# Optimization experiments

Hardware: AMD Instinct MI355X
Metric: run time of the kernel (lower is better)

Reference implementation:

```python
import jax, jax.numpy as jnp
import numpy as np

N_NODES = 100000
N_EDGES = 1600000
IN_CH, HID_CH, OUT_CH = 128, 128, 64


def setup_inputs() -> dict:
    key = jax.random.key(0)
    ks = jax.random.split(key, 9)
    x = jax.random.normal(ks[0], (N_NODES, IN_CH), dtype=jnp.float32)
    edge_index = jax.random.randint(ks[1], (2, N_EDGES), 0, N_NODES, dtype=jnp.int64)
    def glorot(k, shape):
        fan_in = shape[1]
        return jax.random.normal(k, shape, dtype=jnp.float32) / jnp.sqrt(jnp.float32(fan_in))
    return {
        "x": x,
        "edge_index": edge_index,
        "W1_l": glorot(ks[2], (HID_CH, IN_CH)),
        "W1_r": glorot(ks[3], (HID_CH, IN_CH)),
        "b1": jnp.zeros((HID_CH,), jnp.float32),
        "W2_l": glorot(ks[4], (HID_CH, HID_CH)),
        "W2_r": glorot(ks[5], (HID_CH, HID_CH)),
        "b2": jnp.zeros((HID_CH,), jnp.float32),
        "W3_l": glorot(ks[6], (OUT_CH, HID_CH)),
        "W3_r": glorot(ks[7], (OUT_CH, HID_CH)),
        "b3": jnp.zeros((OUT_CH,), jnp.float32),
    }


def _sage_conv(x, src, dst, W_l, W_r, b):
    # PyG SAGEConv (aggr='mean', root_weight=True): out = lin_l(mean_j x_j) + lin_r(x_i)
    n = x.shape[0]
    msg = x[src]                                            # [E, C] gather at source
    agg = jax.ops.segment_sum(msg, dst, num_segments=n)     # [N, C] scatter-sum at dest
    cnt = jax.ops.segment_sum(jnp.ones((src.shape[0],), x.dtype), dst, num_segments=n)
    mean = agg / jnp.maximum(cnt, 1.0)[:, None]             # zero-in-degree nodes -> 0
    return mean @ W_l.T + x @ W_r.T + b


def reference(x, edge_index, W1_l, W1_r, b1, W2_l, W2_r, b2, W3_l, W3_r, b3):
    src, dst = edge_index[0], edge_index[1]
    h = jax.nn.relu(_sage_conv(x, src, dst, W1_l, W1_r, b1))
    # F.dropout with training=False is identity (eval mode)
    h = jax.nn.relu(_sage_conv(h, src, dst, W2_l, W2_r, b2))
    return _sage_conv(h, src, dst, W3_l, W3_r, b3)
```

## Files before the change

kernel.cpp:

```cpp
#include <hip/hip_runtime.h>
#include <hip/hip_bf16.h>
#include <cstddef>
#include <cstdint>

#define NBLK(n, b) (((n) + (b) - 1) / (b))

typedef __attribute__((ext_vector_type(8))) short short8;
typedef __attribute__((ext_vector_type(4))) float f32x4;

__device__ inline unsigned short f2bf(float f) {
  union { float f; unsigned u; } v; v.f = f;
  unsigned u = v.u;
  u += 0x7FFFu + ((u >> 16) & 1u);
  return (unsigned short)(u >> 16);
}
__device__ inline float bflo(unsigned u) { union { unsigned u; float f; } v; v.u = u << 16; return v.f; }
__device__ inline float bfhi(unsigned u) { union { unsigned u; float f; } v; v.u = u & 0xFFFF0000u; return v.f; }

#define BSHIFT 9
#define BSIZE 512
#define CAPSHIFT 14
#define CAP 16384
#define ECHUNK 2048

__global__ __launch_bounds__(256) void k_cast(
    const float* __restrict__ x, unsigned* __restrict__ xb, int N,
    const float* __restrict__ W1l, const float* __restrict__ W1r, unsigned short* __restrict__ Wb1,
    const float* __restrict__ W2l, const float* __restrict__ W2r, unsigned short* __restrict__ Wb2,
    const float* __restrict__ W3l, const float* __restrict__ W3r, unsigned short* __restrict__ Wb3) {
  int t = threadIdx.x;
  int b = blockIdx.x;
  int gCast = (N * 64 + 255) >> 8;
  if (b < gCast) {
    int i = b * 256 + t;
    if (i < N * 64) {
      float2 v = *(const float2*)(x + (size_t)i * 2);
      xb[i] = (unsigned)f2bf(v.x) | ((unsigned)f2bf(v.y) << 16);
    }
    return;
  }
  b -= gCast;
  int ii = b * 256 + t;
  const float *Wl, *Wr; unsigned short* Wb;
  if (ii < 128 * 256) { Wl = W1l; Wr = W1r; Wb = Wb1; }
  else if (ii < 256 * 256) { Wl = W2l; Wr = W2r; Wb = Wb2; ii -= 128 * 256; }
  else { Wl = W3l; Wr = W3r; Wb = Wb3; ii -= 256 * 256; }
  int nrow = ii >> 8, k = ii & 255;
  float v = (k < 128) ? Wr[nrow * 128 + k] : Wl[nrow * 128 + (k - 128)];
  Wb[ii] = f2bf(v);
}

__global__ __launch_bounds__(256) void k_scatter(
    const void* __restrict__ edges, int* __restrict__ bucketCursor,
    unsigned* __restrict__ bucketed, int E, int NB) {
  __shared__ int h[1024];
  __shared__ int base2[1024];
  int t = threadIdx.x;
  int b = blockIdx.x;

  const unsigned* e32 = (const unsigned*)edges;
  int is64 = 1;
#pragma unroll
  for (int i = 0; i < 16; ++i)
    if (e32[2 * i + 1] != 0u) is64 = 0;

  for (int i = t; i < NB; i += 256) h[i] = 0;
  __syncthreads();
  int base_e = b * ECHUNK;
  unsigned key[8];
  int bkt[8];
#pragma unroll
  for (int k = 0; k < 8; ++k) {
    int e = base_e + k * 256 + t;
    bkt[k] = -1;
    if (e < E) {
      int s, d;
      if (is64) {
        s = (int)((const long long*)edges)[e];
        d = (int)((const long long*)edges)[(size_t)E + e];
      } else {
        s = ((const int*)edges)[e];
        d = ((const int*)edges)[(size_t)E + e];
      }
      bkt[k] = d >> BSHIFT;
      key[k] = (unsigned)s | ((unsigned)(d & (BSIZE - 1)) << 17);
      atomicAdd(&h[bkt[k]], 1);
    }
  }
  __syncthreads();
  for (int i = t; i < NB; i += 256) {
    int c = h[i];
    base2[i] = c ? atomicAdd(&bucketCursor[i], c) : 0;
    h[i] = 0;
  }
  __syncthreads();
#pragma unroll
  for (int k = 0; k < 8; ++k) {
    if (bkt[k] >= 0) {
      int r = atomicAdd(&h[bkt[k]], 1);
      int pos = base2[bkt[k]] + r;
      if (pos < CAP)
        bucketed[((size_t)bkt[k] << CAPSHIFT) + pos] = key[k];
    }
  }
}

__global__ __launch_bounds__(256) void k_csr(const unsigned* __restrict__ bucketed,
                                             const int* __restrict__ bucketCursor,
                                             int* __restrict__ rowStart, int* __restrict__ deg,
                                             int* __restrict__ srcSorted, int N, int NB) {
  __shared__ int h[512];
  __shared__ int excl[512];
  __shared__ int sd[256];
  int b = blockIdx.x;
  int t = threadIdx.x;
  int nodeBase = b << BSHIFT;
  int nNode = min(BSIZE, N - nodeBase);
  int cnt = min(bucketCursor[b], CAP);
  size_t s0 = (size_t)b << CAPSHIFT;
  h[t * 2] = 0; h[t * 2 + 1] = 0;
  __syncthreads();
  for (int i = t; i < cnt; i += 256) {
    int ld = bucketed[s0 + i] >> 17;
    atomicAdd(&h[ld], 1);
  }
  __syncthreads();
  int a0 = h[t * 2], a1 = h[t * 2 + 1];
  int s = a0 + a1;
  sd[t] = s;
  __syncthreads();
  for (int off = 1; off < 256; off <<= 1) {
    int xv = (t >= off) ? sd[t - off] : 0;
    __syncthreads();
    sd[t] += xv;
    __syncthreads();
  }
  int run = sd[t] - s;
  excl[t * 2] = run;
  excl[t * 2 + 1] = run + a0;
  if (t * 2 < nNode) {
    rowStart[nodeBase + t * 2] = (int)s0 + run;
    deg[nodeBase + t * 2] = a0;
  }
  if (t * 2 + 1 < nNode) {
    rowStart[nodeBase + t * 2 + 1] = (int)s0 + run + a0;
    deg[nodeBase + t * 2 + 1] = a1;
  }
  h[t * 2] = 0; h[t * 2 + 1] = 0;
  __syncthreads();
  for (int i = t; i < cnt; i += 256) {
    unsigned u = bucketed[s0 + i];
    int ld = u >> 17;
    int r = atomicAdd(&h[ld], 1);
    srcSorted[s0 + excl[ld] + r] = (int)(u & 0x1FFFFu);
  }
}

__global__ void k_aggregate(const unsigned* __restrict__ in, const int* __restrict__ rowStart,
                            const int* __restrict__ deg, const int* __restrict__ srcs,
                            unsigned* __restrict__ mean, int n) {
  int lane = threadIdx.x & 63;
  int w = threadIdx.x >> 6;
  int node = blockIdx.x * 4 + w;
  if (node >= n) return;
  int r0 = rowStart[node];
  int dg = deg[node];
  int r1 = r0 + dg;
  int sub = lane & 15;
  int eg = lane >> 4;
  float acc[8];
#pragma unroll
  for (int k = 0; k < 8; ++k) acc[k] = 0.f;

  for (int base = r0; base < r1; base += 64) {
    int e = base + lane;
    int sv = (e < r1) ? srcs[e] : 0;
    int cnt = min(64, r1 - base);
    int j = 0;
    for (; j + 16 <= cnt; j += 16) {
      int s0 = __shfl(sv, j + eg);
      int s1 = __shfl(sv, j + 4 + eg);
      int s2 = __shfl(sv, j + 8 + eg);
      int s3 = __shfl(sv, j + 12 + eg);
      uint4 u0 = *(const uint4*)(in + (size_t)s0 * 64 + sub * 4);
      uint4 u1 = *(const uint4*)(in + (size_t)s1 * 64 + sub * 4);
      uint4 u2 = *(const uint4*)(in + (size_t)s2 * 64 + sub * 4);
      uint4 u3 = *(const uint4*)(in + (size_t)s3 * 64 + sub * 4);
      acc[0] += bflo(u0.x); acc[1] += bfhi(u0.x);
      acc[2] += bflo(u0.y); acc[3] += bfhi(u0.y);
      acc[4] += bflo(u0.z); acc[5] += bfhi(u0.z);
      acc[6] += bflo(u0.w); acc[7] += bfhi(u0.w);
      acc[0] += bflo(u1.x); acc[1] += bfhi(u1.x);
      acc[2] += bflo(u1.y); acc[3] += bfhi(u1.y);
      acc[4] += bflo(u1.z); acc[5] += bfhi(u1.z);
      acc[6] += bflo(u1.w); acc[7] += bfhi(u1.w);
      acc[0] += bflo(u2.x); acc[1] += bfhi(u2.x);
      acc[2] += bflo(u2.y); acc[3] += bfhi(u2.y);
      acc[4] += bflo(u2.z); acc[5] += bfhi(u2.z);
      acc[6] += bflo(u2.w); acc[7] += bfhi(u2.w);
      acc[0] += bflo(u3.x); acc[1] += bfhi(u3.x);
      acc[2] += bflo(u3.y); acc[3] += bfhi(u3.y);
      acc[4] += bflo(u3.z); acc[5] += bfhi(u3.z);
      acc[6] += bflo(u3.w); acc[7] += bfhi(u3.w);
    }
    for (; j + 8 <= cnt; j += 8) {
      int s0 = __shfl(sv, j + eg);
      int s1 = __shfl(sv, j + 4 + eg);
      uint4 u0 = *(const uint4*)(in + (size_t)s0 * 64 + sub * 4);
      uint4 u1 = *(const uint4*)(in + (size_t)s1 * 64 + sub * 4);
      acc[0] += bflo(u0.x); acc[1] += bfhi(u0.x);
      acc[2] += bflo(u0.y); acc[3] += bfhi(u0.y);
      acc[4] += bflo(u0.z); acc[5] += bfhi(u0.z);
      acc[6] += bflo(u0.w); acc[7] += bfhi(u0.w);
      acc[0] += bflo(u1.x); acc[1] += bfhi(u1.x);
      acc[2] += bflo(u1.y); acc[3] += bfhi(u1.y);
      acc[4] += bflo(u1.z); acc[5] += bfhi(u1.z);
      acc[6] += bflo(u1.w); acc[7] += bfhi(u1.w);
    }
    for (; j < cnt; j += 4) {
      int jj = j + eg;
      int s = __shfl(sv, jj);
      if (jj < cnt) {
        uint4 u = *(const uint4*)(in + (size_t)s * 64 + sub * 4);
        acc[0] += bflo(u.x); acc[1] += bfhi(u.x);
        acc[2] += bflo(u.y); acc[3] += bfhi(u.y);
        acc[4] += bflo(u.z); acc[5] += bfhi(u.z);
        acc[6] += bflo(u.w); acc[7] += bfhi(u.w);
      }
    }
  }

#pragma unroll
  for (int k = 0; k < 8; ++k) {
    acc[k] += __shfl_down(acc[k], 32);
    acc[k] += __shfl_down(acc[k], 16);
  }
  if (eg == 0) {
    float sc = 1.0f / (float)max(dg, 1);
    uint4 o;
    o.x = (unsigned)f2bf(acc[0] * sc) | ((unsigned)f2bf(acc[1] * sc) << 16);
    o.y = (unsigned)f2bf(acc[2] * sc) | ((unsigned)f2bf(acc[3] * sc) << 16);
    o.z = (unsigned)f2bf(acc[4] * sc) | ((unsigned)f2bf(acc[5] * sc) << 16);
    o.w = (unsigned)f2bf(acc[6] * sc) | ((unsigned)f2bf(acc[7] * sc) << 16);
    *(uint4*)(mean + (size_t)node * 64 + sub * 4) = o;
  }
}

template <int H, bool RELU, bool BF16OUT>
__global__ __launch_bounds__(256) void k_gemm(
    const unsigned short* __restrict__ selfB, const unsigned short* __restrict__ meanB,
    const unsigned short* __restrict__ Wb, const float* __restrict__ bias,
    void* __restrict__ outp, int n) {
  constexpr int TN = H / 32;
  int lane = threadIdx.x & 63;
  int w = threadIdx.x >> 6;
  int wr = w & 1, wc = w >> 1;
  int nodeBase = blockIdx.x * 128 + wr * 64;
  int colBase = wc * (H / 2);
  int l15 = lane & 15, quad = lane >> 4;

  f32x4 acc[4][TN];
#pragma unroll
  for (int t = 0; t < 4; ++t)
#pragma unroll
    for (int j = 0; j < TN; ++j) acc[t][j] = (f32x4){0.f, 0.f, 0.f, 0.f};

#pragma unroll
  for (int c = 0; c < 8; ++c) {
    const unsigned short* A = (c < 4) ? selfB : meanB;
    int ko = (c & 3) * 32 + quad * 8;
    short8 af[4], bfr[TN];
#pragma unroll
    for (int t = 0; t < 4; ++t) {
      int row = min(nodeBase + t * 16 + l15, n - 1);
      af[t] = *(const short8*)(A + (size_t)row * 128 + ko);
    }
#pragma unroll
    for (int j = 0; j < TN; ++j) {
      int cn = colBase + j * 16 + l15;
      bfr[j] = *(const short8*)(Wb + (size_t)cn * 256 + c * 32 + quad * 8);
    }
#pragma unroll
    for (int t = 0; t < 4; ++t)
#pragma unroll
      for (int j = 0; j < TN; ++j)
        acc[t][j] = __builtin_amdgcn_mfma_f32_16x16x32_bf16(af[t], bfr[j], acc[t][j], 0, 0, 0);
  }

#pragma unroll
  for (int j = 0; j < TN; ++j) {
    int col = colBase + j * 16 + l15;
    float bv = bias[col];
#pragma unroll
    for (int t = 0; t < 4; ++t) {
#pragma unroll
      for (int r = 0; r < 4; ++r) {
        int row = nodeBase + t * 16 + quad * 4 + r;
        if (row < n) {
          float v = acc[t][j][r] + bv;
          if (RELU) v = fmaxf(v, 0.f);
          if (BF16OUT) ((unsigned short*)outp)[(size_t)row * H + col] = f2bf(v);
          else ((float*)outp)[(size_t)row * H + col] = v;
        }
      }
    }
  }
}

__global__ __launch_bounds__(256) void k_gemm3_both(
    const unsigned short* __restrict__ A,
    const unsigned short* __restrict__ Wb3,
    const float* __restrict__ bias,
    float* __restrict__ outp, unsigned short* __restrict__ y3, int n) {
  int lane = threadIdx.x & 63;
  int w = threadIdx.x >> 6;
  int wr = w & 1, wc = w >> 1;
  int nodeBase = blockIdx.x * 128 + wr * 64;
  int l15 = lane & 15, quad = lane >> 4;
  int woff = wc ? 128 : 0;
  f32x4 acc[4][4];
#pragma unroll
  for (int t = 0; t < 4; ++t)
#pragma unroll
    for (int j = 0; j < 4; ++j) acc[t][j] = (f32x4){0.f, 0.f, 0.f, 0.f};
#pragma unroll
  for (int c = 0; c < 4; ++c) {
    int ko = c * 32 + quad * 8;
    short8 af[4], bfr[4];
#pragma unroll
    for (int t = 0; t < 4; ++t) {
      int row = min(nodeBase + t * 16 + l15, n - 1);
      af[t] = *(const short8*)(A + (size_t)row * 128 + ko);
    }
#pragma unroll
    for (int j = 0; j < 4; ++j) {
      int cn = j * 16 + l15;
      bfr[j] = *(const short8*)(Wb3 + (size_t)cn * 256 + woff + c * 32 + quad * 8);
    }
#pragma unroll
    for (int t = 0; t < 4; ++t)
#pragma unroll
      for (int j = 0; j < 4; ++j)
        acc[t][j] = __builtin_amdgcn_mfma_f32_16x16x32_bf16(af[t], bfr[j], acc[t][j], 0, 0, 0);
  }
#pragma unroll
  for (int j = 0; j < 4; ++j) {
    int col = j * 16 + l15;
    float bv = wc ? 0.f : bias[col];
#pragma unroll
    for (int t = 0; t < 4; ++t) {
#pragma unroll
      for (int r = 0; r < 4; ++r) {
        int row = nodeBase + t * 16 + quad * 4 + r;
        if (row < n) {
          float v = acc[t][j][r] + bv;
          if (wc) y3[(size_t)row * 64 + col] = f2bf(v);
          else outp[(size_t)row * 64 + col] = v;
        }
      }
    }
  }
}

__global__ void k_agg64_add(const unsigned* __restrict__ y3, const int* __restrict__ rowStart,
                            const int* __restrict__ deg, const int* __restrict__ srcs,
                            float* __restrict__ outp, int n) {
  int lane = threadIdx.x & 63;
  int w = threadIdx.x >> 6;
  int node = blockIdx.x * 4 + w;
  if (node >= n) return;
  int dg = deg[node];
  if (dg == 0) return;
  int r0 = rowStart[node];
  int r1 = r0 + dg;
  int sub = lane & 7;
  int eg = lane >> 3;
  float acc[8];
#pragma unroll
  for (int k = 0; k < 8; ++k) acc[k] = 0.f;

  for (int base = r0; base < r1; base += 64) {
    int e = base + lane;
    int sv = (e < r1) ? srcs[e] : 0;
    int cnt = min(64, r1 - base);
    int j = 0;
    for (; j + 16 <= cnt; j += 16) {
      int s0 = __shfl(sv, j + eg);
      int s1 = __shfl(sv, j + 8 + eg);
      uint4 u0 = *(const uint4*)(y3 + (size_t)s0 * 32 + sub * 4);
      uint4 u1 = *(const uint4*)(y3 + (size_t)s1 * 32 + sub * 4);
      acc[0] += bflo(u0.x); acc[1] += bfhi(u0.x);
      acc[2] += bflo(u0.y); acc[3] += bfhi(u0.y);
      acc[4] += bflo(u0.z); acc[5] += bfhi(u0.z);
      acc[6] += bflo(u0.w); acc[7] += bfhi(u0.w);
      acc[0] += bflo(u1.x); acc[1] += bfhi(u1.x);
      acc[2] += bflo(u1.y); acc[3] += bfhi(u1.y);
      acc[4] += bflo(u1.z); acc[5] += bfhi(u1.z);
      acc[6] += bflo(u1.w); acc[7] += bfhi(u1.w);
    }
    for (; j < cnt; j += 8) {
      int jj = j + eg;
      int s = __shfl(sv, jj);
      if (jj < cnt) {
        uint4 u = *(const uint4*)(y3 + (size_t)s * 32 + sub * 4);
        acc[0] += bflo(u.x); acc[1] += bfhi(u.x);
        acc[2] += bflo(u.y); acc[3] += bfhi(u.y);
        acc[4] += bflo(u.z); acc[5] += bfhi(u.z);
        acc[6] += bflo(u.w); acc[7] += bfhi(u.w);
      }
    }
  }

#pragma unroll
  for (int k = 0; k < 8; ++k) {
    acc[k] += __shfl_down(acc[k], 32);
    acc[k] += __shfl_down(acc[k], 16);
    acc[k] += __shfl_down(acc[k], 8);
  }
  if (eg == 0) {
    float sc = 1.0f / (float)dg;
    float* op = outp + (size_t)node * 64 + sub * 8;
    float4 a = *(float4*)op;
    float4 b = *(float4*)(op + 4);
    a.x += acc[0] * sc; a.y += acc[1] * sc; a.z += acc[2] * sc; a.w += acc[3] * sc;
    b.x += acc[4] * sc; b.y += acc[5] * sc; b.z += acc[6] * sc; b.w += acc[7] * sc;
    *(float4*)op = a;
    *(float4*)(op + 4) = b;
  }
}


extern "C" void kernel_launch(void* const* d_in, const int* in_sizes, int n_in,
                              void* d_out, int out_size, void* d_ws, size_t ws_size,
                              hipStream_t stream) {
  (void)n_in; (void)out_size; (void)ws_size;
  const float* x = (const float*)d_in[0];
  const void* edges = d_in[1];
  const float* W1l = (const float*)d_in[2];
  const float* W1r = (const float*)d_in[3];
  const float* b1 = (const float*)d_in[4];
  const float* W2l = (const float*)d_in[5];
  const float* W2r = (const float*)d_in[6];
  const float* b2 = (const float*)d_in[7];
  const float* W3l = (const float*)d_in[8];
  const float* W3r = (const float*)d_in[9];
  const float* b3 = (const float*)d_in[10];
  float* out = (float*)d_out;

  const int N = in_sizes[0] / 128;
  const int E = in_sizes[1] / 2;
  const int NB = (N + BSIZE - 1) >> BSHIFT;

  char* ws = (char*)d_ws;
  size_t off = 0;
  auto alloc = [&](size_t bytes) -> char* {
    char* p = ws + off;
    off = (off + bytes + 255) & ~(size_t)255;
    return p;
  };
  int* bucketCursor = (int*)alloc((size_t)NB * 4);
  unsigned* bucketed = (unsigned*)alloc((size_t)NB * CAP * 4);
  int* rowStart = (int*)alloc((size_t)N * 4);
  int* deg = (int*)alloc((size_t)N * 4);
  int* srcSorted = (int*)alloc((size_t)NB * CAP * 4);
  unsigned short* xb = (unsigned short*)alloc((size_t)N * 128 * 2);
  unsigned short* mean = (unsigned short*)alloc((size_t)N * 128 * 2);
  unsigned short* h1 = (unsigned short*)alloc((size_t)N * 128 * 2);
  unsigned short* h2 = (unsigned short*)alloc((size_t)N * 128 * 2);
  unsigned short* y3 = (unsigned short*)alloc((size_t)N * 64 * 2);
  unsigned short* Wb1 = (unsigned short*)alloc(128 * 256 * 2);
  unsigned short* Wb2 = (unsigned short*)alloc(128 * 256 * 2);
  unsigned short* Wb3 = (unsigned short*)alloc(64 * 256 * 2);

  int gCast = NBLK(N * 64, 256) + 320;
  int gE = NBLK(E, ECHUNK);
  int gAgg = NBLK(N, 4);
  int gGemm = NBLK(N, 128);

  hipMemsetAsync(bucketCursor, 0, (size_t)NB * 4, stream);
  k_cast<<<gCast, 256, 0, stream>>>(x, (unsigned*)xb, N,
                                    W1l, W1r, Wb1, W2l, W2r, Wb2, W3l, W3r, Wb3);
  k_scatter<<<gE, 256, 0, stream>>>(edges, bucketCursor, bucketed, E, NB);
  k_csr<<<NB, 256, 0, stream>>>(bucketed, bucketCursor, rowStart, deg, srcSorted, N, NB);

  k_aggregate<<<gAgg, 256, 0, stream>>>((const unsigned*)xb, rowStart, deg, srcSorted, (unsigned*)mean, N);
  k_gemm<128, true, true><<<gGemm, 256, 0, stream>>>(xb, mean, Wb1, b1, h1, N);
  k_aggregate<<<gAgg, 256, 0, stream>>>((const unsigned*)h1, rowStart, deg, srcSorted, (unsigned*)mean, N);
  k_gemm<128, true, true><<<gGemm, 256, 0, stream>>>(h1, mean, Wb2, b2, h2, N);
  k_gemm3_both<<<gGemm, 256, 0, stream>>>(h2, Wb3, b3, out, y3, N);
  k_agg64_add<<<gAgg, 256, 0, stream>>>((const unsigned*)y3, rowStart, deg, srcSorted, out, N);
}
```

Baseline: 459.0 us.

## Store features in channel-sliced layout and aggregate per slice with thread-per-node

Feature matrices are stored as 8 (or 4) column slices of 16 bf16 channels, each slice contiguous over nodes. Aggregation now launches one block per node range and slice, and each thread pair gathers 32-byte slice rows for one node with 8 loads in flight. The goal is to keep each slice's working set (about 3.2 MB) cache-resident during random gathers and to remove the wave-wide shuffles and reductions. The trade-off is that each thread walks its node's full edge list serially, so load imbalance grows, and the GEMM A-loads and stores become strided across slices.

```diff
diff --git a/kernel.cpp b/kernel.cpp
--- a/kernel.cpp
+++ b/kernel.cpp
@@ -7,6 +7,7 @@
 
 typedef __attribute__((ext_vector_type(8))) short short8;
 typedef __attribute__((ext_vector_type(4))) float f32x4;
+typedef __attribute__((ext_vector_type(2))) float f32x2;
 
 __device__ inline unsigned short f2bf(float f) {
   union { float f; unsigned u; } v; v.f = f;
@@ -23,8 +24,9 @@
 #define CAP 16384
 #define ECHUNK 2048
 
+
 __global__ __launch_bounds__(256) void k_cast(
-    const float* __restrict__ x, unsigned* __restrict__ xb, int N,
+    const float* __restrict__ x, unsigned* __restrict__ xT, int N,
     const float* __restrict__ W1l, const float* __restrict__ W1r, unsigned short* __restrict__ Wb1,
     const float* __restrict__ W2l, const float* __restrict__ W2r, unsigned short* __restrict__ Wb2,
     const float* __restrict__ W3l, const float* __restrict__ W3r, unsigned short* __restrict__ Wb3) {
@@ -35,7 +37,9 @@
     int i = b * 256 + t;
     if (i < N * 64) {
       float2 v = *(const float2*)(x + (size_t)i * 2);
-      xb[i] = (unsigned)f2bf(v.x) | ((unsigned)f2bf(v.y) << 16);
+      int node = i >> 6, j = i & 63;
+      xT[((size_t)(j >> 3) * N + node) * 8 + (j & 7)] =
+          (unsigned)f2bf(v.x) | ((unsigned)f2bf(v.y) << 16);
     }
     return;
   }
@@ -156,101 +160,53 @@
   }
 }
 
-__global__ void k_aggregate(const unsigned* __restrict__ in, const int* __restrict__ rowStart,
-                            const int* __restrict__ deg, const int* __restrict__ srcs,
-                            unsigned* __restrict__ mean, int n) {
-  int lane = threadIdx.x & 63;
-  int w = threadIdx.x >> 6;
-  int node = blockIdx.x * 4 + w;
+__global__ __launch_bounds__(256) void k_agg_slice(
+    const uint4* __restrict__ inT, const int* __restrict__ rowStart,
+    const int* __restrict__ deg, const int* __restrict__ srcs,
+    uint4* __restrict__ outT, int n) {
+  int g = blockIdx.x & 7;
+  int node = ((blockIdx.x >> 3) << 7) + (threadIdx.x >> 1);
+  int h = threadIdx.x & 1;
   if (node >= n) return;
-  int r0 = rowStart[node];
   int dg = deg[node];
-  int r1 = r0 + dg;
-  int sub = lane & 15;
-  int eg = lane >> 4;
-  float acc[8];
-#pragma unroll
-  for (int k = 0; k < 8; ++k) acc[k] = 0.f;
-
-  for (int base = r0; base < r1; base += 64) {
-    int e = base + lane;
-    int sv = (e < r1) ? srcs[e] : 0;
-    int cnt = min(64, r1 - base);
-    int j = 0;
-    for (; j + 16 <= cnt; j += 16) {
-      int s0 = __shfl(sv, j + eg);
-      int s1 = __shfl(sv, j + 4 + eg);
-      int s2 = __shfl(sv, j + 8 + eg);
-      int s3 = __shfl(sv, j + 12 + eg);
-      uint4 u0 = *(const uint4*)(in + (size_t)s0 * 64 + sub * 4);
-      uint4 u1 = *(const uint4*)(in + (size_t)s1 * 64 + sub * 4);
-      uint4 u2 = *(const uint4*)(in + (size_t)s2 * 64 + sub * 4);
-      uint4 u3 = *(const uint4*)(in + (size_t)s3 * 64 + sub * 4);
-      acc[0] += bflo(u0.x); acc[1] += bfhi(u0.x);
-      acc[2] += bflo(u0.y); acc[3] += bfhi(u0.y);
-      acc[4] += bflo(u0.z); acc[5] += bfhi(u0.z);
-      acc[6] += bflo(u0.w); acc[7] += bfhi(u0.w);
-      acc[0] += bflo(u1.x); acc[1] += bfhi(u1.x);
-      acc[2] += bflo(u1.y); acc[3] += bfhi(u1.y);
-      acc[4] += bflo(u1.z); acc[5] += bfhi(u1.z);
-      acc[6] += bflo(u1.w); acc[7] += bfhi(u1.w);
-      acc[0] += bflo(u2.x); acc[1] += bfhi(u2.x);
-      acc[2] += bflo(u2.y); acc[3] += bfhi(u2.y);
-      acc[4] += bflo(u2.z); acc[5] += bfhi(u2.z);
-      acc[6] += bflo(u2.w); acc[7] += bfhi(u2.w);
-      acc[0] += bflo(u3.x); acc[1] += bfhi(u3.x);
-      acc[2] += bflo(u3.y); acc[3] += bfhi(u3.y);
-      acc[4] += bflo(u3.z); acc[5] += bfhi(u3.z);
-      acc[6] += bflo(u3.w); acc[7] += bfhi(u3.w);
-    }
-    for (; j + 8 <= cnt; j += 8) {
-      int s0 = __shfl(sv, j + eg);
-      int s1 = __shfl(sv, j + 4 + eg);
-      uint4 u0 = *(const uint4*)(in + (size_t)s0 * 64 + sub * 4);
-      uint4 u1 = *(const uint4*)(in + (size_t)s1 * 64 + sub * 4);
-      acc[0] += bflo(u0.x); acc[1] += bfhi(u0.x);
-      acc[2] += bflo(u0.y); acc[3] += bfhi(u0.y);
-      acc[4] += bflo(u0.z); acc[5] += bfhi(u0.z);
-      acc[6] += bflo(u0.w); acc[7] += bfhi(u0.w);
-      acc[0] += bflo(u1.x); acc[1] += bfhi(u1.x);
-      acc[2] += bflo(u1.y); acc[3] += bfhi(u1.y);
-      acc[4] += bflo(u1.z); acc[5] += bfhi(u1.z);
-      acc[6] += bflo(u1.w); acc[7] += bfhi(u1.w);
-    }
-    for (; j < cnt; j += 4) {
-      int jj = j + eg;
-      int s = __shfl(sv, jj);
-      if (jj < cnt) {
-        uint4 u = *(const uint4*)(in + (size_t)s * 64 + sub * 4);
-        acc[0] += bflo(u.x); acc[1] += bfhi(u.x);
-        acc[2] += bflo(u.y); acc[3] += bfhi(u.y);
-        acc[4] += bflo(u.z); acc[5] += bfhi(u.z);
-        acc[6] += bflo(u.w); acc[7] += bfhi(u.w);
+  f32x2 acc0 = {0.f, 0.f}, acc1 = {0.f, 0.f}, acc2 = {0.f, 0.f}, acc3 = {0.f, 0.f};
+  const uint4* base = inT + (size_t)g * n * 2 + h;
+  if (dg > 0) {
+    int r0 = rowStart[node];
+    int r1 = r0 + dg;
+    for (int b = r0; b < r1; b += 8) {
+      int s[8];
+      uint4 v[8];
+#pragma unroll
+      for (int i = 0; i < 8; ++i) s[i] = srcs[min(b + i, r1 - 1)] & 0x1FFFF;
+#pragma unroll
+      for (int i = 0; i < 8; ++i) v[i] = base[(size_t)s[i] * 2];
+#pragma unroll
+      for (int i = 0; i < 8; ++i) {
+        if (b + i < r1) {
+          f32x2 t0 = {bflo(v[i].x), bfhi(v[i].x)};
+          f32x2 t1 = {bflo(v[i].y), bfhi(v[i].y)};
+          f32x2 t2 = {bflo(v[i].z), bfhi(v[i].z)};
+          f32x2 t3 = {bflo(v[i].w), bfhi(v[i].w)};
+          acc0 += t0; acc1 += t1; acc2 += t2; acc3 += t3;
+        }
       }
     }
   }
-
-#pragma unroll
-  for (int k = 0; k < 8; ++k) {
-    acc[k] += __shfl_down(acc[k], 32);
-    acc[k] += __shfl_down(acc[k], 16);
-  }
-  if (eg == 0) {
-    float sc = 1.0f / (float)max(dg, 1);
-    uint4 o;
-    o.x = (unsigned)f2bf(acc[0] * sc) | ((unsigned)f2bf(acc[1] * sc) << 16);
-    o.y = (unsigned)f2bf(acc[2] * sc) | ((unsigned)f2bf(acc[3] * sc) << 16);
-    o.z = (unsigned)f2bf(acc[4] * sc) | ((unsigned)f2bf(acc[5] * sc) << 16);
-    o.w = (unsigned)f2bf(acc[6] * sc) | ((unsigned)f2bf(acc[7] * sc) << 16);
-    *(uint4*)(mean + (size_t)node * 64 + sub * 4) = o;
-  }
-}
-
-template <int H, bool RELU, bool BF16OUT>
+  float sc = 1.0f / (float)max(dg, 1);
+  uint4 o;
+  o.x = (unsigned)f2bf(acc0.x * sc) | ((unsigned)f2bf(acc0.y * sc) << 16);
+  o.y = (unsigned)f2bf(acc1.x * sc) | ((unsigned)f2bf(acc1.y * sc) << 16);
+  o.z = (unsigned)f2bf(acc2.x * sc) | ((unsigned)f2bf(acc2.y * sc) << 16);
+  o.w = (unsigned)f2bf(acc3.x * sc) | ((unsigned)f2bf(acc3.y * sc) << 16);
+  outT[((size_t)g * n + node) * 2 + h] = o;
+}
+
+template <int H, bool RELU>
 __global__ __launch_bounds__(256) void k_gemm(
-    const unsigned short* __restrict__ selfB, const unsigned short* __restrict__ meanB,
+    const unsigned short* __restrict__ selfT, const unsigned short* __restrict__ meanT,
     const unsigned short* __restrict__ Wb, const float* __restrict__ bias,
-    void* __restrict__ outp, int n) {
+    unsigned short* __restrict__ outT, int n) {
   constexpr int TN = H / 32;
   int lane = threadIdx.x & 63;
   int w = threadIdx.x >> 6;
@@ -267,13 +223,15 @@
 
 #pragma unroll
   for (int c = 0; c < 8; ++c) {
-    const unsigned short* A = (c < 4) ? selfB : meanB;
+    const unsigned short* A = (c < 4) ? selfT : meanT;
     int ko = (c & 3) * 32 + quad * 8;
+    int gk = ko >> 4;
+    int wo = ko & 15;
     short8 af[4], bfr[TN];
 #pragma unroll
     for (int t = 0; t < 4; ++t) {
       int row = min(nodeBase + t * 16 + l15, n - 1);
-      af[t] = *(const short8*)(A + (size_t)row * 128 + ko);
+      af[t] = *(const short8*)(A + ((size_t)gk * n + row) * 16 + wo);
     }
 #pragma unroll
     for (int j = 0; j < TN; ++j) {
@@ -290,6 +248,7 @@
 #pragma unroll
   for (int j = 0; j < TN; ++j) {
     int col = colBase + j * 16 + l15;
+    int gc = col >> 4;
     float bv = bias[col];
 #pragma unroll
     for (int t = 0; t < 4; ++t) {
@@ -299,8 +258,7 @@
         if (row < n) {
           float v = acc[t][j][r] + bv;
           if (RELU) v = fmaxf(v, 0.f);
-          if (BF16OUT) ((unsigned short*)outp)[(size_t)row * H + col] = f2bf(v);
-          else ((float*)outp)[(size_t)row * H + col] = v;
+          outT[((size_t)gc * n + row) * 16 + l15] = f2bf(v);
         }
       }
     }
@@ -311,7 +269,7 @@
     const unsigned short* __restrict__ A,
     const unsigned short* __restrict__ Wb3,
     const float* __restrict__ bias,
-    float* __restrict__ outp, unsigned short* __restrict__ y3, int n) {
+    float* __restrict__ outp, unsigned short* __restrict__ y3T, int n) {
   int lane = threadIdx.x & 63;
   int w = threadIdx.x >> 6;
   int wr = w & 1, wc = w >> 1;
@@ -326,11 +284,13 @@
 #pragma unroll
   for (int c = 0; c < 4; ++c) {
     int ko = c * 32 + quad * 8;
+    int gk = ko >> 4;
+    int wo = ko & 15;
     short8 af[4], bfr[4];
 #pragma unroll
     for (int t = 0; t < 4; ++t) {
       int row = min(nodeBase + t * 16 + l15, n - 1);
-      af[t] = *(const short8*)(A + (size_t)row * 128 + ko);
+      af[t] = *(const short8*)(A + ((size_t)gk * n + row) * 16 + wo);
     }
 #pragma unroll
     for (int j = 0; j < 4; ++j) {
@@ -354,7 +314,7 @@
         int row = nodeBase + t * 16 + quad * 4 + r;
         if (row < n) {
           float v = acc[t][j][r] + bv;
-          if (wc) y3[(size_t)row * 64 + col] = f2bf(v);
+          if (wc) y3T[((size_t)j * n + row) * 16 + l15] = f2bf(v);
           else outp[(size_t)row * 64 + col] = v;
         }
       }
@@ -362,71 +322,46 @@
   }
 }
 
-__global__ void k_agg64_add(const unsigned* __restrict__ y3, const int* __restrict__ rowStart,
-                            const int* __restrict__ deg, const int* __restrict__ srcs,
-                            float* __restrict__ outp, int n) {
-  int lane = threadIdx.x & 63;
-  int w = threadIdx.x >> 6;
-  int node = blockIdx.x * 4 + w;
+__global__ __launch_bounds__(256) void k_agg64_slice(
+    const uint4* __restrict__ y3T, const int* __restrict__ rowStart,
+    const int* __restrict__ deg, const int* __restrict__ srcs,
+    float* __restrict__ outp, int n) {
+  int g = blockIdx.x & 3;
+  int node = ((blockIdx.x >> 2) << 7) + (threadIdx.x >> 1);
+  int h = threadIdx.x & 1;
   if (node >= n) return;
   int dg = deg[node];
   if (dg == 0) return;
   int r0 = rowStart[node];
   int r1 = r0 + dg;
-  int sub = lane & 7;
-  int eg = lane >> 3;
-  float acc[8];
-#pragma unroll
-  for (int k = 0; k < 8; ++k) acc[k] = 0.f;
-
-  for (int base = r0; base < r1; base += 64) {
-    int e = base + lane;
-    int sv = (e < r1) ? srcs[e] : 0;
-    int cnt = min(64, r1 - base);
-    int j = 0;
-    for (; j + 16 <= cnt; j += 16) {
-      int s0 = __shfl(sv, j + eg);
-      int s1 = __shfl(sv, j + 8 + eg);
-      uint4 u0 = *(const uint4*)(y3 + (size_t)s0 * 32 + sub * 4);
-      uint4 u1 = *(const uint4*)(y3 + (size_t)s1 * 32 + sub * 4);
-      acc[0] += bflo(u0.x); acc[1] += bfhi(u0.x);
-      acc[2] += bflo(u0.y); acc[3] += bfhi(u0.y);
-      acc[4] += bflo(u0.z); acc[5] += bfhi(u0.z);
-      acc[6] += bflo(u0.w); acc[7] += bfhi(u0.w);
-      acc[0] += bflo(u1.x); acc[1] += bfhi(u1.x);
-      acc[2] += bflo(u1.y); acc[3] += bfhi(u1.y);
-      acc[4] += bflo(u1.z); acc[5] += bfhi(u1.z);
-      acc[6] += bflo(u1.w); acc[7] += bfhi(u1.w);
-    }
-    for (; j < cnt; j += 8) {
-      int jj = j + eg;
-      int s = __shfl(sv, jj);
-      if (jj < cnt) {
-        uint4 u = *(const uint4*)(y3 + (size_t)s * 32 + sub * 4);
-        acc[0] += bflo(u.x); acc[1] += bfhi(u.x);
-        acc[2] += bflo(u.y); acc[3] += bfhi(u.y);
-        acc[4] += bflo(u.z); acc[5] += bfhi(u.z);
-        acc[6] += bflo(u.w); acc[7] += bfhi(u.w);
+  f32x2 acc0 = {0.f, 0.f}, acc1 = {0.f, 0.f}, acc2 = {0.f, 0.f}, acc3 = {0.f, 0.f};
+  const uint4* base = y3T + (size_t)g * n * 2 + h;
+  for (int b = r0; b < r1; b += 8) {
+    int s[8];
+    uint4 v[8];
+#pragma unroll
+    for (int i = 0; i < 8; ++i) s[i] = srcs[min(b + i, r1 - 1)] & 0x1FFFF;
+#pragma unroll
+    for (int i = 0; i < 8; ++i) v[i] = base[(size_t)s[i] * 2];
+#pragma unroll
+    for (int i = 0; i < 8; ++i) {
+      if (b + i < r1) {
+        f32x2 t0 = {bflo(v[i].x), bfhi(v[i].x)};
+        f32x2 t1 = {bflo(v[i].y), bfhi(v[i].y)};
+        f32x2 t2 = {bflo(v[i].z), bfhi(v[i].z)};
+        f32x2 t3 = {bflo(v[i].w), bfhi(v[i].w)};
+        acc0 += t0; acc1 += t1; acc2 += t2; acc3 += t3;
       }
     }
   }
-
-#pragma unroll
-  for (int k = 0; k < 8; ++k) {
-    acc[k] += __shfl_down(acc[k], 32);
-    acc[k] += __shfl_down(acc[k], 16);
-    acc[k] += __shfl_down(acc[k], 8);
-  }
-  if (eg == 0) {
-    float sc = 1.0f / (float)dg;
-    float* op = outp + (size_t)node * 64 + sub * 8;
-    float4 a = *(float4*)op;
-    float4 b = *(float4*)(op + 4);
-    a.x += acc[0] * sc; a.y += acc[1] * sc; a.z += acc[2] * sc; a.w += acc[3] * sc;
-    b.x += acc[4] * sc; b.y += acc[5] * sc; b.z += acc[6] * sc; b.w += acc[7] * sc;
-    *(float4*)op = a;
-    *(float4*)(op + 4) = b;
-  }
+  float sc = 1.0f / (float)dg;
+  float* op = outp + (size_t)node * 64 + g * 16 + h * 8;
+  float4 a = *(float4*)op;
+  float4 c = *(float4*)(op + 4);
+  a.x += acc0.x * sc; a.y += acc0.y * sc; a.z += acc1.x * sc; a.w += acc1.y * sc;
+  c.x += acc2.x * sc; c.y += acc2.y * sc; c.z += acc3.x * sc; c.w += acc3.y * sc;
+  *(float4*)op = a;
+  *(float4*)(op + 4) = c;
 }
 
 
@@ -463,30 +398,33 @@
   int* rowStart = (int*)alloc((size_t)N * 4);
   int* deg = (int*)alloc((size_t)N * 4);
   int* srcSorted = (int*)alloc((size_t)NB * CAP * 4);
-  unsigned short* xb = (unsigned short*)alloc((size_t)N * 128 * 2);
-  unsigned short* mean = (unsigned short*)alloc((size_t)N * 128 * 2);
-  unsigned short* h1 = (unsigned short*)alloc((size_t)N * 128 * 2);
-  unsigned short* h2 = (unsigned short*)alloc((size_t)N * 128 * 2);
-  unsigned short* y3 = (unsigned short*)alloc((size_t)N * 64 * 2);
+  unsigned short* xT = (unsigned short*)alloc((size_t)N * 128 * 2);
+  unsigned short* meanT = (unsigned short*)alloc((size_t)N * 128 * 2);
+  unsigned short* h1T = (unsigned short*)alloc((size_t)N * 128 * 2);
+  unsigned short* h2T = (unsigned short*)alloc((size_t)N * 128 * 2);
+  unsigned short* y3T = (unsigned short*)alloc((size_t)N * 64 * 2);
   unsigned short* Wb1 = (unsigned short*)alloc(128 * 256 * 2);
   unsigned short* Wb2 = (unsigned short*)alloc(128 * 256 * 2);
   unsigned short* Wb3 = (unsigned short*)alloc(64 * 256 * 2);
 
   int gCast = NBLK(N * 64, 256) + 320;
   int gE = NBLK(E, ECHUNK);
-  int gAgg = NBLK(N, 4);
+  int gRange = NBLK(N, 128);
   int gGemm = NBLK(N, 128);
 
   hipMemsetAsync(bucketCursor, 0, (size_t)NB * 4, stream);
-  k_cast<<<gCast, 256, 0, stream>>>(x, (unsigned*)xb, N,
+  k_cast<<<gCast, 256, 0, stream>>>(x, (unsigned*)xT, N,
                                     W1l, W1r, Wb1, W2l, W2r, Wb2, W3l, W3r, Wb3);
   k_scatter<<<gE, 256, 0, stream>>>(edges, bucketCursor, bucketed, E, NB);
   k_csr<<<NB, 256, 0, stream>>>(bucketed, bucketCursor, rowStart, deg, srcSorted, N, NB);
 
-  k_aggregate<<<gAgg, 256, 0, stream>>>((const unsigned*)xb, rowStart, deg, srcSorted, (unsigned*)mean, N);
-  k_gemm<128, true, true><<<gGemm, 256, 0, stream>>>(xb, mean, Wb1, b1, h1, N);
-  k_aggregate<<<gAgg, 256, 0, stream>>>((const unsigned*)h1, rowStart, deg, srcSorted, (unsigned*)mean, N);
-  k_gemm<128, true, true><<<gGemm, 256, 0, stream>>>(h1, mean, Wb2, b2, h2, N);
-  k_gemm3_both<<<gGemm, 256, 0, stream>>>(h2, Wb3, b3, out, y3, N);
-  k_agg64_add<<<gAgg, 256, 0, stream>>>((const unsigned*)y3, rowStart, deg, srcSorted, out, N);
-}
+  k_agg_slice<<<gRange * 8, 256, 0, stream>>>((const uint4*)xT, rowStart, deg, srcSorted,
+                                              (uint4*)meanT, N);
+  k_gemm<128, true><<<gGemm, 256, 0, stream>>>(xT, meanT, Wb1, b1, h1T, N);
+  k_agg_slice<<<gRange * 8, 256, 0, stream>>>((const uint4*)h1T, rowStart, deg, srcSorted,
+                                              (uint4*)meanT, N);
+  k_gemm<128, true><<<gGemm, 256, 0, stream>>>(h1T, meanT, Wb2, b2, h2T, N);
+  k_gemm3_both<<<gGemm, 256, 0, stream>>>(h2T, Wb3, b3, out, y3T, N);
+  k_agg64_slice<<<gRange * 4, 256, 0, stream>>>((const uint4*)y3T, rowStart, deg, srcSorted,
+                                                out, N);
+}
```

After: 525.0 us. +14.4%, slower.

## Degree-sort nodes per bucket and aggregate two nodes per wavefront

Applied to the files above, without the earlier changes.

The CSR build kernel now also emits a permutation that orders nodes within each 512-node bucket by in-degree (capped at 63) using a shared-memory counting sort. The aggregation kernels read this permutation and let each wavefront process two nodes of similar degree together, issuing their gathers interleaved. This is meant to cut load imbalance and raise memory-level parallelism. The cost is an extra indirection, more registers per wave, and scattered output writes in permuted order.

```diff
diff --git a/kernel.cpp b/kernel.cpp
--- a/kernel.cpp
+++ b/kernel.cpp
@@ -16,6 +16,14 @@
 }
 __device__ inline float bflo(unsigned u) { union { unsigned u; float f; } v; v.u = u << 16; return v.f; }
 __device__ inline float bfhi(unsigned u) { union { unsigned u; float f; } v; v.u = u & 0xFFFF0000u; return v.f; }
+
+__device__ inline void add8(float* a, uint4 v) {
+  a[0] += bflo(v.x); a[1] += bfhi(v.x);
+  a[2] += bflo(v.y); a[3] += bfhi(v.y);
+  a[4] += bflo(v.z); a[5] += bfhi(v.z);
+  a[6] += bflo(v.w); a[7] += bfhi(v.w);
+}
+
 
 #define BSHIFT 9
 #define BSIZE 512
@@ -108,7 +116,8 @@
 __global__ __launch_bounds__(256) void k_csr(const unsigned* __restrict__ bucketed,
                                              const int* __restrict__ bucketCursor,
                                              int* __restrict__ rowStart, int* __restrict__ deg,
-                                             int* __restrict__ srcSorted, int N, int NB) {
+                                             int* __restrict__ srcSorted, int* __restrict__ perm,
+                                             int N, int NB) {
   __shared__ int h[512];
   __shared__ int excl[512];
   __shared__ int sd[256];
@@ -154,95 +163,146 @@
     int r = atomicAdd(&h[ld], 1);
     srcSorted[s0 + excl[ld] + r] = (int)(u & 0x1FFFFu);
   }
+  __syncthreads();
+  if (t < 64) sd[t] = 0;
+  __syncthreads();
+  if (t * 2 < nNode) atomicAdd(&sd[min(a0, 63)], 1);
+  if (t * 2 + 1 < nNode) atomicAdd(&sd[min(a1, 63)], 1);
+  __syncthreads();
+  if (t == 0) {
+    int r2 = 0;
+    for (int i = 0; i < 64; ++i) { int c = sd[i]; excl[i] = r2; r2 += c; }
+  }
+  __syncthreads();
+  if (t * 2 < nNode) {
+    int p = atomicAdd(&excl[min(a0, 63)], 1);
+    perm[nodeBase + p] = nodeBase + t * 2;
+  }
+  if (t * 2 + 1 < nNode) {
+    int p = atomicAdd(&excl[min(a1, 63)], 1);
+    perm[nodeBase + p] = nodeBase + t * 2 + 1;
+  }
 }
 
 __global__ void k_aggregate(const unsigned* __restrict__ in, const int* __restrict__ rowStart,
                             const int* __restrict__ deg, const int* __restrict__ srcs,
-                            unsigned* __restrict__ mean, int n) {
+                            const int* __restrict__ perm, unsigned* __restrict__ mean, int n) {
   int lane = threadIdx.x & 63;
   int w = threadIdx.x >> 6;
-  int node = blockIdx.x * 4 + w;
-  if (node >= n) return;
-  int r0 = rowStart[node];
-  int dg = deg[node];
-  int r1 = r0 + dg;
+  int i0 = blockIdx.x * 8 + w * 2;
+  bool vA = i0 < n, vB = i0 + 1 < n;
+  int nA = vA ? perm[i0] : 0;
+  int nB = vB ? perm[i0 + 1] : 0;
+  int dga = vA ? deg[nA] : 0;
+  int dgb = vB ? deg[nB] : 0;
+  int r0a = vA ? rowStart[nA] : 0;
+  int r0b = vB ? rowStart[nB] : 0;
   int sub = lane & 15;
   int eg = lane >> 4;
-  float acc[8];
-#pragma unroll
-  for (int k = 0; k < 8; ++k) acc[k] = 0.f;
-
-  for (int base = r0; base < r1; base += 64) {
-    int e = base + lane;
-    int sv = (e < r1) ? srcs[e] : 0;
-    int cnt = min(64, r1 - base);
+  float accA[8], accB[8];
+#pragma unroll
+  for (int k = 0; k < 8; ++k) { accA[k] = 0.f; accB[k] = 0.f; }
+
+  int mx = max(dga, dgb);
+  for (int base = 0; base < mx; base += 64) {
+    int cA = min(64, dga - base);
+    int cB = min(64, dgb - base);
+    int svA = (lane < cA) ? srcs[r0a + base + lane] : 0;
+    int svB = (lane < cB) ? srcs[r0b + base + lane] : 0;
     int j = 0;
-    for (; j + 16 <= cnt; j += 16) {
-      int s0 = __shfl(sv, j + eg);
-      int s1 = __shfl(sv, j + 4 + eg);
-      int s2 = __shfl(sv, j + 8 + eg);
-      int s3 = __shfl(sv, j + 12 + eg);
-      uint4 u0 = *(const uint4*)(in + (size_t)s0 * 64 + sub * 4);
-      uint4 u1 = *(const uint4*)(in + (size_t)s1 * 64 + sub * 4);
-      uint4 u2 = *(const uint4*)(in + (size_t)s2 * 64 + sub * 4);
-      uint4 u3 = *(const uint4*)(in + (size_t)s3 * 64 + sub * 4);
-      acc[0] += bflo(u0.x); acc[1] += bfhi(u0.x);
-      acc[2] += bflo(u0.y); acc[3] += bfhi(u0.y);
-      acc[4] += bflo(u0.z); acc[5] += bfhi(u0.z);
-      acc[6] += bflo(u0.w); acc[7] += bfhi(u0.w);
-      acc[0] += bflo(u1.x); acc[1] += bfhi(u1.x);
-      acc[2] += bflo(u1.y); acc[3] += bfhi(u1.y);
-      acc[4] += bflo(u1.z); acc[5] += bfhi(u1.z);
-      acc[6] += bflo(u1.w); acc[7] += bfhi(u1.w);
-      acc[0] += bflo(u2.x); acc[1] += bfhi(u2.x);
-      acc[2] += bflo(u2.y); acc[3] += bfhi(u2.y);
-      acc[4] += bflo(u2.z); acc[5] += bfhi(u2.z);
-      acc[6] += bflo(u2.w); acc[7] += bfhi(u2.w);
-      acc[0] += bflo(u3.x); acc[1] += bfhi(u3.x);
-      acc[2] += bflo(u3.y); acc[3] += bfhi(u3.y);
-      acc[4] += bflo(u3.z); acc[5] += bfhi(u3.z);
-      acc[6] += bflo(u3.w); acc[7] += bfhi(u3.w);
-    }
-    for (; j + 8 <= cnt; j += 8) {
-      int s0 = __shfl(sv, j + eg);
-      int s1 = __shfl(sv, j + 4 + eg);
-      uint4 u0 = *(const uint4*)(in + (size_t)s0 * 64 + sub * 4);
-      uint4 u1 = *(const uint4*)(in + (size_t)s1 * 64 + sub * 4);
-      acc[0] += bflo(u0.x); acc[1] += bfhi(u0.x);
-      acc[2] += bflo(u0.y); acc[3] += bfhi(u0.y);
-      acc[4] += bflo(u0.z); acc[5] += bfhi(u0.z);
-      acc[6] += bflo(u0.w); acc[7] += bfhi(u0.w);
-      acc[0] += bflo(u1.x); acc[1] += bfhi(u1.x);
-      acc[2] += bflo(u1.y); acc[3] += bfhi(u1.y);
-      acc[4] += bflo(u1.z); acc[5] += bfhi(u1.z);
-      acc[6] += bflo(u1.w); acc[7] += bfhi(u1.w);
-    }
-    for (; j < cnt; j += 4) {
-      int jj = j + eg;
-      int s = __shfl(sv, jj);
-      if (jj < cnt) {
-        uint4 u = *(const uint4*)(in + (size_t)s * 64 + sub * 4);
-        acc[0] += bflo(u.x); acc[1] += bfhi(u.x);
-        acc[2] += bflo(u.y); acc[3] += bfhi(u.y);
-        acc[4] += bflo(u.z); acc[5] += bfhi(u.z);
-        acc[6] += bflo(u.w); acc[7] += bfhi(u.w);
+    int cM = min(cA, cB);
+    for (; j + 16 <= cM; j += 16) {
+      int a0 = __shfl(svA, j + eg), a1 = __shfl(svA, j + 4 + eg);
+      int a2 = __shfl(svA, j + 8 + eg), a3 = __shfl(svA, j + 12 + eg);
+      int b0 = __shfl(svB, j + eg), b1 = __shfl(svB, j + 4 + eg);
+      int b2 = __shfl(svB, j + 8 + eg), b3 = __shfl(svB, j + 12 + eg);
+      uint4 uA0 = *(const uint4*)(in + (size_t)a0 * 64 + sub * 4);
+      uint4 uA1 = *(const uint4*)(in + (size_t)a1 * 64 + sub * 4);
+      uint4 uA2 = *(const uint4*)(in + (size_t)a2 * 64 + sub * 4);
+      uint4 uA3 = *(const uint4*)(in + (size_t)a3 * 64 + sub * 4);
+      uint4 uB0 = *(const uint4*)(in + (size_t)b0 * 64 + sub * 4);
+      uint4 uB1 = *(const uint4*)(in + (size_t)b1 * 64 + sub * 4);
+      uint4 uB2 = *(const uint4*)(in + (size_t)b2 * 64 + sub * 4);
+      uint4 uB3 = *(const uint4*)(in + (size_t)b3 * 64 + sub * 4);
+      add8(accA, uA0); add8(accA, uA1); add8(accA, uA2); add8(accA, uA3);
+      add8(accB, uB0); add8(accB, uB1); add8(accB, uB2); add8(accB, uB3);
+    }
+    int ja = j;
+    for (; ja + 16 <= cA; ja += 16) {
+      int a0 = __shfl(svA, ja + eg), a1 = __shfl(svA, ja + 4 + eg);
+      int a2 = __shfl(svA, ja + 8 + eg), a3 = __shfl(svA, ja + 12 + eg);
+      uint4 u0 = *(const uint4*)(in + (size_t)a0 * 64 + sub * 4);
+      uint4 u1 = *(const uint4*)(in + (size_t)a1 * 64 + sub * 4);
+      uint4 u2 = *(const uint4*)(in + (size_t)a2 * 64 + sub * 4);
+      uint4 u3 = *(const uint4*)(in + (size_t)a3 * 64 + sub * 4);
+      add8(accA, u0); add8(accA, u1); add8(accA, u2); add8(accA, u3);
+    }
+    for (; ja + 8 <= cA; ja += 8) {
+      int a0 = __shfl(svA, ja + eg), a1 = __shfl(svA, ja + 4 + eg);
+      uint4 u0 = *(const uint4*)(in + (size_t)a0 * 64 + sub * 4);
+      uint4 u1 = *(const uint4*)(in + (size_t)a1 * 64 + sub * 4);
+      add8(accA, u0); add8(accA, u1);
+    }
+    for (; ja < cA; ja += 4) {
+      int jj = ja + eg;
+      int s2 = __shfl(svA, jj);
+      if (jj < cA) {
+        uint4 u = *(const uint4*)(in + (size_t)s2 * 64 + sub * 4);
+        add8(accA, u);
+      }
+    }
+    int jb = j;
+    for (; jb + 16 <= cB; jb += 16) {
+      int b0 = __shfl(svB, jb + eg), b1 = __shfl(svB, jb + 4 + eg);
+      int b2 = __shfl(svB, jb + 8 + eg), b3 = __shfl(svB, jb + 12 + eg);
+      uint4 u0 = *(const uint4*)(in + (size_t)b0 * 64 + sub * 4);
+      uint4 u1 = *(const uint4*)(in + (size_t)b1 * 64 + sub * 4);
+      uint4 u2 = *(const uint4*)(in + (size_t)b2 * 64 + sub * 4);
+      uint4 u3 = *(const uint4*)(in + (size_t)b3 * 64 + sub * 4);
+      add8(accB, u0); add8(accB, u1); add8(accB, u2); add8(accB, u3);
+    }
+    for (; jb + 8 <= cB; jb += 8) {
+      int b0 = __shfl(svB, jb + eg), b1 = __shfl(svB, jb + 4 + eg);
+      uint4 u0 = *(const uint4*)(in + (size_t)b0 * 64 + sub * 4);
+      uint4 u1 = *(const uint4*)(in + (size_t)b1 * 64 + sub * 4);
+      add8(accB, u0); add8(accB, u1);
+    }
+    for (; jb < cB; jb += 4) {
+      int jj = jb + eg;
+      int s2 = __shfl(svB, jj);
+      if (jj < cB) {
+        uint4 u = *(const uint4*)(in + (size_t)s2 * 64 + sub * 4);
+        add8(accB, u);
       }
     }
   }
 
 #pragma unroll
   for (int k = 0; k < 8; ++k) {
-    acc[k] += __shfl_down(acc[k], 32);
-    acc[k] += __shfl_down(acc[k], 16);
+    accA[k] += __shfl_down(accA[k], 32);
+    accA[k] += __shfl_down(accA[k], 16);
+    accB[k] += __shfl_down(accB[k], 32);
+    accB[k] += __shfl_down(accB[k], 16);
   }
   if (eg == 0) {
-    float sc = 1.0f / (float)max(dg, 1);
-    uint4 o;
-    o.x = (unsigned)f2bf(acc[0] * sc) | ((unsigned)f2bf(acc[1] * sc) << 16);
-    o.y = (unsigned)f2bf(acc[2] * sc) | ((unsigned)f2bf(acc[3] * sc) << 16);
-    o.z = (unsigned)f2bf(acc[4] * sc) | ((unsigned)f2bf(acc[5] * sc) << 16);
-    o.w = (unsigned)f2bf(acc[6] * sc) | ((unsigned)f2bf(acc[7] * sc) << 16);
-    *(uint4*)(mean + (size_t)node * 64 + sub * 4) = o;
+    if (vA) {
+      float sc = 1.0f / (float)max(dga, 1);
+      uint4 o;
+      o.x = (unsigned)f2bf(accA[0] * sc) | ((unsigned)f2bf(accA[1] * sc) << 16);
+      o.y = (unsigned)f2bf(accA[2] * sc) | ((unsigned)f2bf(accA[3] * sc) << 16);
+      o.z = (unsigned)f2bf(accA[4] * sc) | ((unsigned)f2bf(accA[5] * sc) << 16);
+      o.w = (unsigned)f2bf(accA[6] * sc) | ((unsigned)f2bf(accA[7] * sc) << 16);
+      *(uint4*)(mean + (size_t)nA * 64 + sub * 4) = o;
+    }
+    if (vB) {
+      float sc = 1.0f / (float)max(dgb, 1);
+      uint4 o;
+      o.x = (unsigned)f2bf(accB[0] * sc) | ((unsigned)f2bf(accB[1] * sc) << 16);
+      o.y = (unsigned)f2bf(accB[2] * sc) | ((unsigned)f2bf(accB[3] * sc) << 16);
+      o.z = (unsigned)f2bf(accB[4] * sc) | ((unsigned)f2bf(accB[5] * sc) << 16);
+      o.w = (unsigned)f2bf(accB[6] * sc) | ((unsigned)f2bf(accB[7] * sc) << 16);
+      *(uint4*)(mean + (size_t)nB * 64 + sub * 4) = o;
+    }
   }
 }
 
@@ -364,68 +424,103 @@
 
 __global__ void k_agg64_add(const unsigned* __restrict__ y3, const int* __restrict__ rowStart,
                             const int* __restrict__ deg, const int* __restrict__ srcs,
-                            float* __restrict__ outp, int n) {
+                            const int* __restrict__ perm, float* __restrict__ outp, int n) {
   int lane = threadIdx.x & 63;
   int w = threadIdx.x >> 6;
-  int node = blockIdx.x * 4 + w;
-  if (node >= n) return;
-  int dg = deg[node];
-  if (dg == 0) return;
-  int r0 = rowStart[node];
-  int r1 = r0 + dg;
+  int i0 = blockIdx.x * 8 + w * 2;
+  bool vA = i0 < n, vB = i0 + 1 < n;
+  int nA = vA ? perm[i0] : 0;
+  int nB = vB ? perm[i0 + 1] : 0;
+  int dga = vA ? deg[nA] : 0;
+  int dgb = vB ? deg[nB] : 0;
+  int r0a = vA ? rowStart[nA] : 0;
+  int r0b = vB ? rowStart[nB] : 0;
   int sub = lane & 7;
   int eg = lane >> 3;
-  float acc[8];
-#pragma unroll
-  for (int k = 0; k < 8; ++k) acc[k] = 0.f;
-
-  for (int base = r0; base < r1; base += 64) {
-    int e = base + lane;
-    int sv = (e < r1) ? srcs[e] : 0;
-    int cnt = min(64, r1 - base);
+  float accA[8], accB[8];
+#pragma unroll
+  for (int k = 0; k < 8; ++k) { accA[k] = 0.f; accB[k] = 0.f; }
+
+  int mx = max(dga, dgb);
+  for (int base = 0; base < mx; base += 64) {
+    int cA = min(64, dga - base);
+    int cB = min(64, dgb - base);
+    int svA = (lane < cA) ? srcs[r0a + base + lane] : 0;
+    int svB = (lane < cB) ? srcs[r0b + base + lane] : 0;
     int j = 0;
-    for (; j + 16 <= cnt; j += 16) {
-      int s0 = __shfl(sv, j + eg);
-      int s1 = __shfl(sv, j + 8 + eg);
-      uint4 u0 = *(const uint4*)(y3 + (size_t)s0 * 32 + sub * 4);
-      uint4 u1 = *(const uint4*)(y3 + (size_t)s1 * 32 + sub * 4);
-      acc[0] += bflo(u0.x); acc[1] += bfhi(u0.x);
-      acc[2] += bflo(u0.y); acc[3] += bfhi(u0.y);
-      acc[4] += bflo(u0.z); acc[5] += bfhi(u0.z);
-      acc[6] += bflo(u0.w); acc[7] += bfhi(u0.w);
-      acc[0] += bflo(u1.x); acc[1] += bfhi(u1.x);
-      acc[2] += bflo(u1.y); acc[3] += bfhi(u1.y);
-      acc[4] += bflo(u1.z); acc[5] += bfhi(u1.z);
-      acc[6] += bflo(u1.w); acc[7] += bfhi(u1.w);
-    }
-    for (; j < cnt; j += 8) {
-      int jj = j + eg;
-      int s = __shfl(sv, jj);
-      if (jj < cnt) {
-        uint4 u = *(const uint4*)(y3 + (size_t)s * 32 + sub * 4);
-        acc[0] += bflo(u.x); acc[1] += bfhi(u.x);
-        acc[2] += bflo(u.y); acc[3] += bfhi(u.y);
-        acc[4] += bflo(u.z); acc[5] += bfhi(u.z);
-        acc[6] += bflo(u.w); acc[7] += bfhi(u.w);
+    int cM = min(cA, cB);
+    for (; j + 16 <= cM; j += 16) {
+      int a0 = __shfl(svA, j + eg), a1 = __shfl(svA, j + 8 + eg);
+      int b0 = __shfl(svB, j + eg), b1 = __shfl(svB, j + 8 + eg);
+      uint4 uA0 = *(const uint4*)(y3 + (size_t)a0 * 32 + sub * 4);
+      uint4 uA1 = *(const uint4*)(y3 + (size_t)a1 * 32 + sub * 4);
+      uint4 uB0 = *(const uint4*)(y3 + (size_t)b0 * 32 + sub * 4);
+      uint4 uB1 = *(const uint4*)(y3 + (size_t)b1 * 32 + sub * 4);
+      add8(accA, uA0); add8(accA, uA1);
+      add8(accB, uB0); add8(accB, uB1);
+    }
+    int ja = j;
+    for (; ja + 16 <= cA; ja += 16) {
+      int a0 = __shfl(svA, ja + eg), a1 = __shfl(svA, ja + 8 + eg);
+      uint4 u0 = *(const uint4*)(y3 + (size_t)a0 * 32 + sub * 4);
+      uint4 u1 = *(const uint4*)(y3 + (size_t)a1 * 32 + sub * 4);
+      add8(accA, u0); add8(accA, u1);
+    }
+    for (; ja < cA; ja += 8) {
+      int jj = ja + eg;
+      int s2 = __shfl(svA, jj);
+      if (jj < cA) {
+        uint4 u = *(const uint4*)(y3 + (size_t)s2 * 32 + sub * 4);
+        add8(accA, u);
+      }
+    }
+    int jb = j;
+    for (; jb + 16 <= cB; jb += 16) {
+      int b0 = __shfl(svB, jb + eg), b1 = __shfl(svB, jb + 8 + eg);
+      uint4 u0 = *(const uint4*)(y3 + (size_t)b0 * 32 + sub * 4);
+      uint4 u1 = *(const uint4*)(y3 + (size_t)b1 * 32 + sub * 4);
+      add8(accB, u0); add8(accB, u1);
+    }
+    for (; jb < cB; jb += 8) {
+      int jj = jb + eg;
+      int s2 = __shfl(svB, jj);
+      if (jj < cB) {
+        uint4 u = *(const uint4*)(y3 + (size_t)s2 * 32 + sub * 4);
+        add8(accB, u);
       }
     }
   }
 
 #pragma unroll
   for (int k = 0; k < 8; ++k) {
-    acc[k] += __shfl_down(acc[k], 32);
-    acc[k] += __shfl_down(acc[k], 16);
-    acc[k] += __shfl_down(acc[k], 8);
+    accA[k] += __shfl_down(accA[k], 32);
+    accA[k] += __shfl_down(accA[k], 16);
+    accA[k] += __shfl_down(accA[k], 8);
+    accB[k] += __shfl_down(accB[k], 32);
+    accB[k] += __shfl_down(accB[k], 16);
+    accB[k] += __shfl_down(accB[k], 8);
   }
   if (eg == 0) {
-    float sc = 1.0f / (float)dg;
-    float* op = outp + (size_t)node * 64 + sub * 8;
-    float4 a = *(float4*)op;
-    float4 b = *(float4*)(op + 4);
-    a.x += acc[0] * sc; a.y += acc[1] * sc; a.z += acc[2] * sc; a.w += acc[3] * sc;
-    b.x += acc[4] * sc; b.y += acc[5] * sc; b.z += acc[6] * sc; b.w += acc[7] * sc;
-    *(float4*)op = a;
-    *(float4*)(op + 4) = b;
+    if (vA && dga > 0) {
+      float sc = 1.0f / (float)dga;
+      float* op = outp + (size_t)nA * 64 + sub * 8;
+      float4 a = *(float4*)op;
+      float4 b = *(float4*)(op + 4);
+      a.x += accA[0] * sc; a.y += accA[1] * sc; a.z += accA[2] * sc; a.w += accA[3] * sc;
+      b.x += accA[4] * sc; b.y += accA[5] * sc; b.z += accA[6] * sc; b.w += accA[7] * sc;
+      *(float4*)op = a;
+      *(float4*)(op + 4) = b;
+    }
+    if (vB && dgb > 0) {
+      float sc = 1.0f / (float)dgb;
+      float* op = outp + (size_t)nB * 64 + sub * 8;
+      float4 a = *(float4*)op;
+      float4 b = *(float4*)(op + 4);
+      a.x += accB[0] * sc; a.y += accB[1] * sc; a.z += accB[2] * sc; a.w += accB[3] * sc;
+      b.x += accB[4] * sc; b.y += accB[5] * sc; b.z += accB[6] * sc; b.w += accB[7] * sc;
+      *(float4*)op = a;
+      *(float4*)(op + 4) = b;
+    }
   }
 }
 
@@ -462,6 +557,7 @@
   unsigned* bucketed = (unsigned*)alloc((size_t)NB * CAP * 4);
   int* rowStart = (int*)alloc((size_t)N * 4);
   int* deg = (int*)alloc((size_t)N * 4);
+  int* perm = (int*)alloc((size_t)N * 4);
   int* srcSorted = (int*)alloc((size_t)NB * CAP * 4);
   unsigned short* xb = (unsigned short*)alloc((size_t)N * 128 * 2);
   unsigned short* mean = (unsigned short*)alloc((size_t)N * 128 * 2);
@@ -474,19 +570,22 @@
 
   int gCast = NBLK(N * 64, 256) + 320;
   int gE = NBLK(E, ECHUNK);
-  int gAgg = NBLK(N, 4);
+  int gAgg = NBLK(N, 8);
   int gGemm = NBLK(N, 128);
 
   hipMemsetAsync(bucketCursor, 0, (size_t)NB * 4, stream);
   k_cast<<<gCast, 256, 0, stream>>>(x, (unsigned*)xb, N,
                                     W1l, W1r, Wb1, W2l, W2r, Wb2, W3l, W3r, Wb3);
   k_scatter<<<gE, 256, 0, stream>>>(edges, bucketCursor, bucketed, E, NB);
-  k_csr<<<NB, 256, 0, stream>>>(bucketed, bucketCursor, rowStart, deg, srcSorted, N, NB);
-
-  k_aggregate<<<gAgg, 256, 0, stream>>>((const unsigned*)xb, rowStart, deg, srcSorted, (unsigned*)mean, N);
+  k_csr<<<NB, 256, 0, stream>>>(bucketed, bucketCursor, rowStart, deg, srcSorted, perm, N, NB);
+
+  k_aggregate<<<gAgg, 256, 0, stream>>>((const unsigned*)xb, rowStart, deg, srcSorted, perm,
+                                        (unsigned*)mean, N);
   k_gemm<128, true, true><<<gGemm, 256, 0, stream>>>(xb, mean, Wb1, b1, h1, N);
-  k_aggregate<<<gAgg, 256, 0, stream>>>((const unsigned*)h1, rowStart, deg, srcSorted, (unsigned*)mean, N);
+  k_aggregate<<<gAgg, 256, 0, stream>>>((const unsigned*)h1, rowStart, deg, srcSorted, perm,
+                                        (unsigned*)mean, N);
   k_gemm<128, true, true><<<gGemm, 256, 0, stream>>>(h1, mean, Wb2, b2, h2, N);
   k_gemm3_both<<<gGemm, 256, 0, stream>>>(h2, Wb3, b3, out, y3, N);
-  k_agg64_add<<<gAgg, 256, 0, stream>>>((const unsigned*)y3, rowStart, deg, srcSorted, out, N);
-}
+  k_agg64_add<<<gAgg, 256, 0, stream>>>((const unsigned*)y3, rowStart, deg, srcSorted, perm,
+                                        out, N);
+}
```

New measurement: 478.8 us. 1.04x slower.
